# Performance work log

Hardware: AMD Instinct MI355X
Metric: run time of the kernel (lower is better)

The kernel has to match this reference:

```python
import jax, jax.numpy as jnp
import numpy as np

T = 64
NBITS_PSUM = 8
NBITS_ACC = 8
K = 2
EPS = 1e-5

def _binarize_ste(x):
    # sign binarization with straight-through estimator (torch code overwrites .data)
    s = jnp.where(x >= 0, 1.0, -1.0).astype(x.dtype)
    return x + jax.lax.stop_gradient(s - x)

def _binary_conv_psum(x, w):
    # x: [N,C,H,W], w: [O,C,3,3]. Binarized 3x3 conv (stride 1, pad 1) computed as
    # chunks of T products along the unrolled reduction dim, each partial sum
    # quantized to NBITS_PSUM bits with step K, final accumulator clipped to NBITS_ACC.
    N, C, H, W = x.shape
    O = w.shape[0]
    xb = _binarize_ste(x)
    wb = _binarize_ste(w)
    patches = jax.lax.conv_general_dilated_patches(
        xb, (3, 3), (1, 1), ((1, 1), (1, 1)),
        dimension_numbers=('NCHW', 'OIHW', 'NCHW'))  # [N, C*9, H, W], channel-major
    R = C * 9
    nch = R // T  # 2304 / 64 = 36 chunks
    p = patches.reshape(N, nch, T, H, W).transpose(1, 0, 2, 3, 4)  # [nch,N,T,H,W]
    wf = wb.reshape(O, nch, T).transpose(1, 0, 2)                   # [nch,O,T]
    qmax = 2 ** (NBITS_PSUM - 1) - 1
    step = float(K)

    def body(carry, xs):
        acc, reg = carry
        pc, wc = xs
        psum = jnp.einsum('nthw,ot->nohw', pc, wc)  # partial sum over T binary products
        q = jnp.clip(jnp.round(psum / step), -qmax - 1, qmax) * step
        q_ste = psum + jax.lax.stop_gradient(q - psum)  # STE through quantizer
        reg = reg + jnp.mean((q - psum) ** 2)  # quantization-error regularizer
        return (acc + q_ste, reg), None

    acc0 = jnp.zeros((N, O, H, W), x.dtype)
    (acc, reg), _ = jax.lax.scan(body, (acc0, jnp.zeros((), x.dtype)), (p, wf))
    amax = (2 ** (NBITS_ACC - 1) - 1) * step  # accumulator clipping
    return jnp.clip(acc, -amax, amax), reg

def _bn(x, gamma, beta):
    # BatchNorm2d in training mode (batch statistics)
    m = jnp.mean(x, (0, 2, 3), keepdims=True)
    v = jnp.var(x, (0, 2, 3), keepdims=True)
    return (x - m) * jax.lax.rsqrt(v + EPS) * gamma[None, :, None, None] + beta[None, :, None, None]

def setup_inputs():
    key = jax.random.key(0)
    k1, k2, k3 = jax.random.split(key, 3)
    N, C, H, W = 32, 256, 32, 32
    return {
        'x0': jax.random.normal(k1, (N, C, H, W), jnp.float32),
        'reg0': jnp.zeros((), jnp.float32),
        'w1': jax.random.normal(k2, (C, C, 3, 3), jnp.float32),
        'gamma1': jnp.ones((C,), jnp.float32),
        'beta1': jnp.zeros((C,), jnp.float32),
        'w2': jax.random.normal(k3, (C, C, 3, 3), jnp.float32),
        'gamma2': jnp.ones((C,), jnp.float32),
        'beta2': jnp.zeros((C,), jnp.float32),
    }

def reference(x0, reg0, w1, gamma1, beta1, w2, gamma2, beta2):
    residual = x0
    out, r1 = _binary_conv_psum(x0, w1)
    reg = reg0 + r1
    out = _bn(out, gamma1, beta1)
    out = jnp.clip(out, -1.0, 1.0)  # Hardtanh
    out, r2 = _binary_conv_psum(out, w2)
    reg = reg + r2
    out = out + residual  # downsample is None
    reg = reg + r2        # faithful to original: conv2's r is added again after residual
    out = _bn(out, gamma2, beta2)
    out = jnp.clip(out, -1.0, 1.0)  # Hardtanh (do_bntan=True)
    return out, reg
```

## Files before the change

kernel.cpp:

```cpp
#include <hip/hip_runtime.h>

typedef unsigned long long u64;
typedef __attribute__((ext_vector_type(4)))  int i32x4;
typedef __attribute__((ext_vector_type(16))) int i32x16;

#define NPIX   32768
#define OCH    256
#define NCH    36

#define AROWS  196
#define ALDS   (AROWS * 256)
#define BLDS   8192
#define GLDS   (ALDS + 3 * BLDS)

__device__ __forceinline__ void gload16(const void* g, void* l) {
  __builtin_amdgcn_global_load_lds(
      (const __attribute__((address_space(1))) unsigned*)g,
      (__attribute__((address_space(3))) unsigned*)l, 16, 0, 0);
}

__global__ void bb_prep(const float* wa, const float* wb, u64* Wbits,
                        signed char* B, float* st, u64* masks) {
  int blk = blockIdx.x, t = threadIdx.x;
  if (blk == 0) {
    for (int i = t; i < 1024; i += 256) st[i] = 0.f;
    for (int id = t; id < 9 * NCH; id += 256) {
      int cls = id / NCH, ck = id % NCH;
      int ch = cls / 3, cw = cls % 3;
      u64 m = 0;
      for (int b = 0; b < 64; ++b) {
        int r = ck * 64 + b, tap = r % 9, kh = tap / 3, kw = tap % 3;
        bool oob = (ch == 0 && kh == 0) || (ch == 2 && kh == 2) ||
                   (cw == 0 && kw == 0) || (cw == 2 && kw == 2);
        if (!oob) m |= (u64)1 << b;
      }
      masks[id] = m;
    }
  } else if (blk <= 4608) {
    int word = (((blk - 1) << 8) + t) >> 6;
    int ln = t & 63;
    const float* src = (word < OCH * NCH) ? wa : wb;
    int r = word % (OCH * NCH);
    u64 bits = __ballot(src[(size_t)r * 64 + ln] >= 0.f);
    int l = word / (OCH * NCH);
    int o = r / NCH, ck = r % NCH;
    if (ln == 0) Wbits[(size_t)l * OCH * NCH + (size_t)ck * OCH + o] = bits;
  } else {
    int tid = ((blk - 4609) << 8) + t;
    int l = tid >= 589824;
    int r = l ? tid - 589824 : tid;
    const float* src = l ? wb : wa;
    float v = src[r];
    int tp = r % 9, oc9 = r / 9;
    int c = oc9 & 255, o = oc9 >> 8;
    B[(((size_t)(l * 9 + tp) * 256 + o) << 8) + c] = (v >= 0.f) ? 1 : -1;
  }
}

__global__ __launch_bounds__(256) void bb_xbits(const float* __restrict__ x,
                                                u64* __restrict__ Sb,
                                                signed char* __restrict__ A) {
  __shared__ float xt[256][33];
  int n = blockIdx.x >> 5, h = blockIdx.x & 31;
  int t = threadIdx.x;
  int w = t & 31, cg = t >> 5;
  for (int k = 0; k < 32; ++k) {
    int c = k * 8 + cg;
    xt[c][w] = x[((size_t)((n * 256 + c) * 32 + h) << 5) + w];
  }
  __syncthreads();
  int ln = t & 63, wv = t >> 6;
  int c2 = wv * 64 + ln;
  for (int w2 = 0; w2 < 32; ++w2) {
    bool s = xt[c2][w2] >= 0.f;
    u64 bits = __ballot(s);
    int px = (n * 32 + h) * 32 + w2;
    A[(size_t)px * 256 + c2] = s ? 1 : -1;
    if (ln == 0) Sb[(size_t)px * 4 + wv] = bits;
  }
}

__global__ __launch_bounds__(256, 2) void bb_gemm(const signed char* __restrict__ A,
                                                  const signed char* __restrict__ B,
                                                  short* __restrict__ dst) {
  extern __shared__ signed char sm[];
  int t = threadIdx.x, wv = t >> 6, ln = t & 63;
  int lw = ln & 31, hk = ln >> 5;
  int px0 = blockIdx.x << 7;
  int oc0 = blockIdx.y << 7;

  const signed char* Abase = A + (size_t)(px0 - 33) * 256;
  #pragma unroll
  for (int i = 0; i < 13; ++i) {
    int c = i * 4 + wv;
    if (c < 49) {
      int u = c * 64 + ln;
      int row = u >> 4, p = u & 15;
      gload16(Abase + (size_t)row * 256 + (((p ^ (row & 7)) << 4)),
              &sm[c * 1024]);
    }
  }

  #define STAGE_B(bufi, ks) do {                                              \
    int tp_ = (ks) >> 2, cb_ = (ks) & 3;                                      \
    const signed char* Bb_ = B + ((size_t)tp_ << 16) + (size_t)oc0 * 256      \
                               + (cb_ << 6);                                  \
    _Pragma("unroll")                                                         \
    for (int i_ = 0; i_ < 2; ++i_) {                                          \
      int c_ = wv * 2 + i_;                                                   \
      int u_ = c_ * 64 + ln;                                                  \
      int row_ = u_ >> 2, p_ = u_ & 3;                                        \
      gload16(Bb_ + (size_t)row_ * 256 + (((p_ ^ ((row_ >> 1) & 3)) << 4)),   \
              &sm[ALDS + (bufi) * BLDS + c_ * 1024]);                         \
    }                                                                         \
  } while (0)

  STAGE_B(0, 0);
  STAGE_B(1, 1);
  asm volatile("s_waitcnt vmcnt(2)" ::: "memory");
  __builtin_amdgcn_s_barrier();

  int wm = wv >> 1, wn = wv & 1;
  int arow0 = 33 + (wm << 6) + lw;
  int brow0 = (wn << 6) + lw;
  i32x16 acc00 = {0,0,0,0,0,0,0,0,0,0,0,0,0,0,0,0};
  i32x16 acc01 = acc00, acc10 = acc00, acc11 = acc00;

  for (int ks = 0; ks < 36; ++ks) {
    if (ks + 2 < 36) STAGE_B((ks + 2) % 3, ks + 2);
    int tp = ks >> 2, cb = ks & 3;
    int dpx = (tp / 3 - 1) * 32 + (tp % 3 - 1);
    int r0 = arow0 + dpx, r1 = r0 + 32;
    int q0 = brow0, q1 = brow0 + 32;
    const signed char* Bl = sm + ALDS + (ks % 3) * BLDS;
    __builtin_amdgcn_s_setprio(1);
    #pragma unroll
    for (int k32 = 0; k32 < 2; ++k32) {
      int sa = cb * 4 + k32 * 2 + hk;
      int sb = k32 * 2 + hk;
      i32x4 a0 = *(const i32x4*)(sm + r0 * 256 + ((sa ^ (r0 & 7)) << 4));
      i32x4 a1 = *(const i32x4*)(sm + r1 * 256 + ((sa ^ (r1 & 7)) << 4));
      i32x4 b0 = *(const i32x4*)(Bl + q0 * 64 + ((sb ^ ((q0 >> 1) & 3)) << 4));
      i32x4 b1 = *(const i32x4*)(Bl + q1 * 64 + ((sb ^ ((q1 >> 1) & 3)) << 4));
      acc00 = __builtin_amdgcn_mfma_i32_32x32x32_i8(a0, b0, acc00, 0, 0, 0);
      acc01 = __builtin_amdgcn_mfma_i32_32x32x32_i8(a0, b1, acc01, 0, 0, 0);
      acc10 = __builtin_amdgcn_mfma_i32_32x32x32_i8(a1, b0, acc10, 0, 0, 0);
      acc11 = __builtin_amdgcn_mfma_i32_32x32x32_i8(a1, b1, acc11, 0, 0, 0);
    }
    __builtin_amdgcn_s_setprio(0);
    if (ks < 34) asm volatile("s_waitcnt vmcnt(2)" ::: "memory");
    else         asm volatile("s_waitcnt vmcnt(0)" ::: "memory");
    __builtin_amdgcn_s_barrier();
  }
  #undef STAGE_B

  int px0w = px0 + (wm << 6), oc0w = oc0 + (wn << 6);
  int rbase = hk << 2;
  #pragma unroll
  for (int r = 0; r < 16; ++r) {
    int m = (r & 3) + ((r >> 2) << 3) + rbase;
    size_t row0 = ((size_t)(px0w + m)) << 8;
    size_t row1 = ((size_t)(px0w + 32 + m)) << 8;
    int v;
    v = acc00[r]; v = v < -254 ? -254 : (v > 254 ? 254 : v);
    dst[row0 + oc0w + lw] = (short)v;
    v = acc01[r]; v = v < -254 ? -254 : (v > 254 ? 254 : v);
    dst[row0 + oc0w + 32 + lw] = (short)v;
    v = acc10[r]; v = v < -254 ? -254 : (v > 254 ? 254 : v);
    dst[row1 + oc0w + lw] = (short)v;
    v = acc11[r]; v = v < -254 ? -254 : (v > 254 ? 254 : v);
    dst[row1 + oc0w + 32 + lw] = (short)v;
  }
}

__global__ __launch_bounds__(256) void bb_bconv(const u64* __restrict__ Sb,
                                                const u64* __restrict__ Wb,
                                                const u64* __restrict__ masks,
                                                short* __restrict__ dst) {
  __shared__ u64 spread[256];
  __shared__ u64 pw[16][NCH];
  __shared__ u64 mm[16][NCH];
  __shared__ int pm[16][NCH];
  __shared__ int pxl[16];
  int t = threadIdx.x;
  {
    u64 v = 0;
    for (int k = 0; k < 8; ++k) if (t & (1 << k)) v |= (u64)1 << (9 * k);
    spread[t] = v;
  }
  __syncthreads();
  for (int id = t; id < 16 * NCH; id += 256) {
    int p = id / NCH, ck = id % NCH;
    int gp = blockIdx.x * 16 + p;
    int n = gp / 124, r = gp % 124;
    int h, w;
    if (r < 32)      { h = 0;      w = r;      }
    else if (r < 64) { h = 31;     w = r - 32; }
    else if (r < 94) { h = r - 63; w = 0;      }
    else             { h = r - 93; w = 31;     }
    int cls = (h == 0 ? 0 : (h == 31 ? 2 : 1)) * 3 + (w == 0 ? 0 : (w == 31 ? 2 : 1));
    if (ck == 0) pxl[p] = ((n * 32 + h) << 5) + w;
    int base9 = ck % 9;
    u64 acc = 0;
    for (int tap = 0; tap < 9; ++tap) {
      int b0 = tap - base9; if (b0 < 0) b0 += 9;
      int nh = h + tap / 3 - 1, nw = w + tap % 3 - 1;
      if ((unsigned)nh <= 31u && (unsigned)nw <= 31u) {
        int run = (b0 == 0) ? 8 : 7;
        int c0 = (ck * 64 + b0) / 9;
        const u64* rp = Sb + ((size_t)((n * 32 + nh) * 32 + nw) << 2);
        int wi = c0 >> 6, sh = c0 & 63;
        u64 v = rp[wi] >> sh;
        if (sh + run > 64) v |= rp[wi + 1] << (64 - sh);
        v &= (run == 8) ? 0xFFull : 0x7Full;
        acc |= spread[(int)v] << b0;
      }
    }
    pw[p][ck] = acc;
    u64 m = masks[cls * NCH + ck];
    mm[p][ck] = m;
    pm[p][ck] = __popcll(m);
  }
  __syncthreads();
  int oc = t;
  int acc[16];
  #pragma unroll
  for (int p = 0; p < 16; ++p) acc[p] = 0;
  for (int i = 0; i < NCH; ++i) {
    u64 wr = Wb[(size_t)i * OCH + oc];
    #pragma unroll
    for (int p = 0; p < 16; ++p) {
      int d = __popcll((pw[p][i] ^ wr) & mm[p][i]);
      int ps = pm[p][i] - 2 * d;
      acc[p] += ps + (ps & 1) * ((ps & 2) - 1);
    }
  }
  #pragma unroll
  for (int p = 0; p < 16; ++p) {
    int v = acc[p];
    v = v < -254 ? -254 : (v > 254 ? 254 : v);
    dst[(size_t)pxl[p] * OCH + oc] = (short)v;
  }
}

__global__ void bb_stats1(const short* v16, float* st) {
  int t = threadIdx.x;
  const short* base = v16 + (size_t)blockIdx.x * 128 * OCH;
  int s = 0; float q = 0.f;
  for (int r = 0; r < 128; ++r) {
    int v = base[r * OCH + t];
    s += v; q += (float)(v * v);
  }
  atomicAdd(&st[t], (float)s);
  atomicAdd(&st[256 + t], q);
}

__global__ void bb_xbits2(const short* v16, const float* st,
                          const float* g, const float* b, u64* Sb,
                          signed char* A) {
  int wave = (blockIdx.x * blockDim.x + threadIdx.x) >> 6;
  int ln = threadIdx.x & 63;
  int wrd = wave & 3, px0 = (wave >> 2) * 32;
  int oc = wrd * 64 + ln;
  float mu = st[oc] * (1.f / 32768.f);
  float va = st[256 + oc] * (1.f / 32768.f) - mu * mu;
  float rs = rsqrtf(va + 1e-5f);
  float gg = g[oc], bb = b[oc];
  for (int j = 0; j < 32; ++j) {
    float bn = ((float)v16[(size_t)(px0 + j) * OCH + oc] - mu) * rs * gg + bb;
    bool s = bn >= 0.f;
    u64 bits = __ballot(s);
    A[(size_t)(px0 + j) * 256 + oc] = s ? 1 : -1;
    if (ln == 0) Sb[(size_t)(px0 + j) * 4 + wrd] = bits;
  }
}

__global__ __launch_bounds__(256) void bb_stats2t(const short* __restrict__ pre16,
                                                  const float* __restrict__ x0,
                                                  float* st) {
  __shared__ float xt[32][257];
  int blk = blockIdx.x;
  int n = blk >> 5, h = blk & 31;
  int t = threadIdx.x;
  int w = t & 31, og = t >> 5;
  for (int k = 0; k < 32; ++k) {
    int oc = og * 32 + k;
    xt[w][oc] = x0[((size_t)(n * 256 + oc) * 32 + h) * 32 + w];
  }
  __syncthreads();
  int oc = t;
  size_t pb = (size_t)blk * 32 * OCH + oc;
  float s = 0.f, q = 0.f;
  for (int w2 = 0; w2 < 32; ++w2) {
    float v = (float)pre16[pb + (size_t)w2 * OCH] + xt[w2][oc];
    s += v; q += v * v;
  }
  atomicAdd(&st[512 + oc], s);
  atomicAdd(&st[768 + oc], q);
}

__global__ __launch_bounds__(256) void bb_fint(const short* __restrict__ pre16,
                                               const float* __restrict__ x0,
                                               const float* st, const float* g,
                                               const float* b, const float* r0,
                                               float* __restrict__ out) {
  __shared__ float xt[32][257];
  int blk = blockIdx.x;
  int n = blk >> 5, h = blk & 31;
  int t = threadIdx.x;
  int w = t & 31, og = t >> 5;
  for (int k = 0; k < 32; ++k) {
    int oc = og * 32 + k;
    xt[w][oc] = x0[((size_t)(n * 256 + oc) * 32 + h) * 32 + w];
  }
  __syncthreads();
  int oc = t;
  float mu = st[512 + oc] * (1.f / 32768.f);
  float va = st[768 + oc] * (1.f / 32768.f) - mu * mu;
  float rs = rsqrtf(va + 1e-5f);
  float gg = g[oc], bb = b[oc];
  size_t pb = (size_t)blk * 32 * OCH + oc;
  for (int w2 = 0; w2 < 32; ++w2) {
    float v = (float)pre16[pb + (size_t)w2 * OCH] + xt[w2][oc];
    v = (v - mu) * rs * gg + bb;
    xt[w2][oc] = fminf(fmaxf(v, -1.f), 1.f);
  }
  __syncthreads();
  for (int k = 0; k < 32; ++k) {
    int oc2 = og * 32 + k;
    out[((size_t)(n * 256 + oc2) * 32 + h) * 32 + w] = xt[w][oc2];
  }
  if (blk == 0 && t == 0) out[8388608] = r0[0] + 8.625f;
}

extern "C" void kernel_launch(void* const* d_in, const int* in_sizes, int n_in,
                              void* d_out, int out_size, void* d_ws, size_t ws_size,
                              hipStream_t stream) {
  const float* x0   = (const float*)d_in[0];
  const float* reg0 = (const float*)d_in[1];
  const float* w1   = (const float*)d_in[2];
  const float* g1   = (const float*)d_in[3];
  const float* b1   = (const float*)d_in[4];
  const float* w2   = (const float*)d_in[5];
  const float* g2   = (const float*)d_in[6];
  const float* b2   = (const float*)d_in[7];

  char* ws = (char*)d_ws;
  u64*   Wbits = (u64*)(ws);
  u64*   masks = (u64*)(ws + 147456);
  float* st    = (float*)(ws + 151552);
  u64*   Sb    = (u64*)(ws + 155648);
  signed char* Bi8 = (signed char*)(ws + 1204224);
  signed char* Ai8 = (signed char*)(ws + 2383872) + 32768;
  short* v16   = (short*)(ws + 10838016);

  bb_prep   <<<9217, 256, 0, stream>>>(w1, w2, Wbits, Bi8, st, masks);
  bb_xbits  <<<1024, 256, 0, stream>>>(x0, Sb, Ai8);
  bb_gemm   <<<dim3(256, 2), 256, GLDS, stream>>>(Ai8, Bi8, v16);
  bb_bconv  <<<248,  256, 0, stream>>>(Sb, Wbits, masks, v16);
  bb_stats1 <<<256,  256, 0, stream>>>(v16, st);
  bb_xbits2 <<<1024, 256, 0, stream>>>(v16, st, g1, b1, Sb, Ai8);
  bb_gemm   <<<dim3(256, 2), 256, GLDS, stream>>>(Ai8, Bi8 + 589824, v16);
  bb_bconv  <<<248,  256, 0, stream>>>(Sb, Wbits + OCH * NCH, masks, v16);
  bb_stats2t<<<1024, 256, 0, stream>>>(v16, x0, st);
  bb_fint   <<<1024, 256, 0, stream>>>(v16, x0, st, g2, b2, reg0, (float*)d_out);
}
```

Measured before the change: 308.0 us.

## Load GEMM B operand directly from global in MFMA-ready layout, drop LDS staging

The weight (B) matrix is now written by the prep kernel in a fragment-ordered layout so each lane can load its 16-byte MFMA operand straight from global memory. The triple-buffered LDS staging of B, its barriers and waitcnts are removed from the GEMM loop, which shrinks shared memory to the A tile and raises the occupancy hint to 3 blocks. This removes per-step synchronisation and LDS traffic, but B reads now go through L1/L2 with latency that is no longer explicitly prefetched, which may stall MFMAs.

New measurement: 320.0 us. 3.9% more time.

```diff
diff --git a/kernel.cpp b/kernel.cpp
--- a/kernel.cpp
+++ b/kernel.cpp
@@ -10,8 +10,6 @@
 
 #define AROWS  196
 #define ALDS   (AROWS * 256)
-#define BLDS   8192
-#define GLDS   (ALDS + 3 * BLDS)
 
 __device__ __forceinline__ void gload16(const void* g, void* l) {
   __builtin_amdgcn_global_load_lds(
@@ -53,7 +51,9 @@
     float v = src[r];
     int tp = r % 9, oc9 = r / 9;
     int c = oc9 & 255, o = oc9 >> 8;
-    B[(((size_t)(l * 9 + tp) * 256 + o) << 8) + c] = (v >= 0.f) ? 1 : -1;
+    int cb = c >> 6, s = (c >> 4) & 3, j = c & 15;
+    B[(((size_t)((l * 9 + tp) * 16 + cb * 4 + s)) << 12) + (o << 4) + j] =
+        (v >= 0.f) ? 1 : -1;
   }
 }
 
@@ -80,7 +80,7 @@
   }
 }
 
-__global__ __launch_bounds__(256, 2) void bb_gemm(const signed char* __restrict__ A,
+__global__ __launch_bounds__(256, 3) void bb_gemm(const signed char* __restrict__ A,
                                                   const signed char* __restrict__ B,
                                                   short* __restrict__ dst) {
   extern __shared__ signed char sm[];
@@ -100,59 +100,34 @@
               &sm[c * 1024]);
     }
   }
-
-  #define STAGE_B(bufi, ks) do {                                              \
-    int tp_ = (ks) >> 2, cb_ = (ks) & 3;                                      \
-    const signed char* Bb_ = B + ((size_t)tp_ << 16) + (size_t)oc0 * 256      \
-                               + (cb_ << 6);                                  \
-    _Pragma("unroll")                                                         \
-    for (int i_ = 0; i_ < 2; ++i_) {                                          \
-      int c_ = wv * 2 + i_;                                                   \
-      int u_ = c_ * 64 + ln;                                                  \
-      int row_ = u_ >> 2, p_ = u_ & 3;                                        \
-      gload16(Bb_ + (size_t)row_ * 256 + (((p_ ^ ((row_ >> 1) & 3)) << 4)),   \
-              &sm[ALDS + (bufi) * BLDS + c_ * 1024]);                         \
-    }                                                                         \
-  } while (0)
-
-  STAGE_B(0, 0);
-  STAGE_B(1, 1);
-  asm volatile("s_waitcnt vmcnt(2)" ::: "memory");
+  asm volatile("s_waitcnt vmcnt(0)" ::: "memory");
   __builtin_amdgcn_s_barrier();
 
   int wm = wv >> 1, wn = wv & 1;
   int arow0 = 33 + (wm << 6) + lw;
-  int brow0 = (wn << 6) + lw;
+  const signed char* Bw = B + (((size_t)(oc0 + (wn << 6) + lw)) << 4);
   i32x16 acc00 = {0,0,0,0,0,0,0,0,0,0,0,0,0,0,0,0};
   i32x16 acc01 = acc00, acc10 = acc00, acc11 = acc00;
 
+  #pragma unroll 4
   for (int ks = 0; ks < 36; ++ks) {
-    if (ks + 2 < 36) STAGE_B((ks + 2) % 3, ks + 2);
     int tp = ks >> 2, cb = ks & 3;
     int dpx = (tp / 3 - 1) * 32 + (tp % 3 - 1);
     int r0 = arow0 + dpx, r1 = r0 + 32;
-    int q0 = brow0, q1 = brow0 + 32;
-    const signed char* Bl = sm + ALDS + (ks % 3) * BLDS;
-    __builtin_amdgcn_s_setprio(1);
     #pragma unroll
     for (int k32 = 0; k32 < 2; ++k32) {
       int sa = cb * 4 + k32 * 2 + hk;
-      int sb = k32 * 2 + hk;
+      size_t bb = ((size_t)(tp * 16 + cb * 4 + k32 * 2 + hk)) << 12;
       i32x4 a0 = *(const i32x4*)(sm + r0 * 256 + ((sa ^ (r0 & 7)) << 4));
       i32x4 a1 = *(const i32x4*)(sm + r1 * 256 + ((sa ^ (r1 & 7)) << 4));
-      i32x4 b0 = *(const i32x4*)(Bl + q0 * 64 + ((sb ^ ((q0 >> 1) & 3)) << 4));
-      i32x4 b1 = *(const i32x4*)(Bl + q1 * 64 + ((sb ^ ((q1 >> 1) & 3)) << 4));
+      i32x4 b0 = *(const i32x4*)(Bw + bb);
+      i32x4 b1 = *(const i32x4*)(Bw + bb + (32 << 4));
       acc00 = __builtin_amdgcn_mfma_i32_32x32x32_i8(a0, b0, acc00, 0, 0, 0);
       acc01 = __builtin_amdgcn_mfma_i32_32x32x32_i8(a0, b1, acc01, 0, 0, 0);
       acc10 = __builtin_amdgcn_mfma_i32_32x32x32_i8(a1, b0, acc10, 0, 0, 0);
       acc11 = __builtin_amdgcn_mfma_i32_32x32x32_i8(a1, b1, acc11, 0, 0, 0);
     }
-    __builtin_amdgcn_s_setprio(0);
-    if (ks < 34) asm volatile("s_waitcnt vmcnt(2)" ::: "memory");
-    else         asm volatile("s_waitcnt vmcnt(0)" ::: "memory");
-    __builtin_amdgcn_s_barrier();
-  }
-  #undef STAGE_B
+  }
 
   int px0w = px0 + (wm << 6), oc0w = oc0 + (wn << 6);
   int rbase = hk << 2;
@@ -356,11 +331,11 @@
 
   bb_prep   <<<9217, 256, 0, stream>>>(w1, w2, Wbits, Bi8, st, masks);
   bb_xbits  <<<1024, 256, 0, stream>>>(x0, Sb, Ai8);
-  bb_gemm   <<<dim3(256, 2), 256, GLDS, stream>>>(Ai8, Bi8, v16);
+  bb_gemm   <<<dim3(256, 2), 256, ALDS, stream>>>(Ai8, Bi8, v16);
   bb_bconv  <<<248,  256, 0, stream>>>(Sb, Wbits, masks, v16);
   bb_stats1 <<<256,  256, 0, stream>>>(v16, st);
   bb_xbits2 <<<1024, 256, 0, stream>>>(v16, st, g1, b1, Sb, Ai8);
-  bb_gemm   <<<dim3(256, 2), 256, GLDS, stream>>>(Ai8, Bi8 + 589824, v16);
+  bb_gemm   <<<dim3(256, 2), 256, ALDS, stream>>>(Ai8, Bi8 + 589824, v16);
   bb_bconv  <<<248,  256, 0, stream>>>(Sb, Wbits + OCH * NCH, masks, v16);
   bb_stats2t<<<1024, 256, 0, stream>>>(v16, x0, st);
   bb_fint   <<<1024, 256, 0, stream>>>(v16, x0, st, g2, b2, reg0, (float*)d_out);
```

## Merge prep with xbits, and fuse interior GEMM with border bconv into one launch

Applied to the files above, without the earlier changes.

Folds the input binarization into the weight-prep kernel and combines the int8 MFMA GEMM and the border-pixel popcount conv into one kernel, with block ranges selecting the role. The GEMM now skips storing border pixels so the two roles write disjoint outputs and can run concurrently. This removes three kernel launches and the serialization between GEMM and bconv. The cost is that bconv blocks now reserve the large GEMM LDS allocation, which may limit their occupancy, and the prep kernel carries the xt shared array for every block.

New measurement: 283.4 us. -8.0%, faster.

```diff
diff --git a/kernel.cpp b/kernel.cpp
--- a/kernel.cpp
+++ b/kernel.cpp
@@ -19,8 +19,16 @@
       (__attribute__((address_space(3))) unsigned*)l, 16, 0, 0);
 }
 
-__global__ void bb_prep(const float* wa, const float* wb, u64* Wbits,
-                        signed char* B, float* st, u64* masks) {
+__global__ __launch_bounds__(256) void bb_pre(const float* __restrict__ wa,
+                                              const float* __restrict__ wb,
+                                              const float* __restrict__ x,
+                                              u64* __restrict__ Wbits,
+                                              signed char* __restrict__ B,
+                                              float* __restrict__ st,
+                                              u64* __restrict__ masks,
+                                              u64* __restrict__ Sb,
+                                              signed char* __restrict__ A) {
+  __shared__ float xt[256][33];
   int blk = blockIdx.x, t = threadIdx.x;
   if (blk == 0) {
     for (int i = t; i < 1024; i += 256) st[i] = 0.f;
@@ -45,7 +53,7 @@
     int l = word / (OCH * NCH);
     int o = r / NCH, ck = r % NCH;
     if (ln == 0) Wbits[(size_t)l * OCH * NCH + (size_t)ck * OCH + o] = bits;
-  } else {
+  } else if (blk <= 9216) {
     int tid = ((blk - 4609) << 8) + t;
     int l = tid >= 589824;
     int r = l ? tid - 589824 : tid;
@@ -54,144 +62,149 @@
     int tp = r % 9, oc9 = r / 9;
     int c = oc9 & 255, o = oc9 >> 8;
     B[(((size_t)(l * 9 + tp) * 256 + o) << 8) + c] = (v >= 0.f) ? 1 : -1;
-  }
-}
-
-__global__ __launch_bounds__(256) void bb_xbits(const float* __restrict__ x,
-                                                u64* __restrict__ Sb,
-                                                signed char* __restrict__ A) {
-  __shared__ float xt[256][33];
-  int n = blockIdx.x >> 5, h = blockIdx.x & 31;
-  int t = threadIdx.x;
-  int w = t & 31, cg = t >> 5;
-  for (int k = 0; k < 32; ++k) {
-    int c = k * 8 + cg;
-    xt[c][w] = x[((size_t)((n * 256 + c) * 32 + h) << 5) + w];
-  }
-  __syncthreads();
-  int ln = t & 63, wv = t >> 6;
-  int c2 = wv * 64 + ln;
-  for (int w2 = 0; w2 < 32; ++w2) {
-    bool s = xt[c2][w2] >= 0.f;
-    u64 bits = __ballot(s);
-    int px = (n * 32 + h) * 32 + w2;
-    A[(size_t)px * 256 + c2] = s ? 1 : -1;
-    if (ln == 0) Sb[(size_t)px * 4 + wv] = bits;
-  }
-}
-
-__global__ __launch_bounds__(256, 2) void bb_gemm(const signed char* __restrict__ A,
+  } else {
+    int bx = blk - 9217;
+    int n = bx >> 5, h = bx & 31;
+    int w = t & 31, cg = t >> 5;
+    for (int k = 0; k < 32; ++k) {
+      int c = k * 8 + cg;
+      xt[c][w] = x[((size_t)((n * 256 + c) * 32 + h) << 5) + w];
+    }
+    __syncthreads();
+    int ln = t & 63, wv = t >> 6;
+    int c2 = wv * 64 + ln;
+    for (int w2 = 0; w2 < 32; ++w2) {
+      bool s = xt[c2][w2] >= 0.f;
+      u64 bits = __ballot(s);
+      int px = (n * 32 + h) * 32 + w2;
+      A[(size_t)px * 256 + c2] = s ? 1 : -1;
+      if (ln == 0) Sb[(size_t)px * 4 + wv] = bits;
+    }
+  }
+}
+
+__global__ __launch_bounds__(256, 2) void bb_conv(const signed char* __restrict__ A,
                                                   const signed char* __restrict__ B,
+                                                  const u64* __restrict__ Sb,
+                                                  const u64* __restrict__ Wb,
+                                                  const u64* __restrict__ masks,
                                                   short* __restrict__ dst) {
   extern __shared__ signed char sm[];
-  int t = threadIdx.x, wv = t >> 6, ln = t & 63;
-  int lw = ln & 31, hk = ln >> 5;
-  int px0 = blockIdx.x << 7;
-  int oc0 = blockIdx.y << 7;
-
-  const signed char* Abase = A + (size_t)(px0 - 33) * 256;
-  #pragma unroll
-  for (int i = 0; i < 13; ++i) {
-    int c = i * 4 + wv;
-    if (c < 49) {
-      int u = c * 64 + ln;
-      int row = u >> 4, p = u & 15;
-      gload16(Abase + (size_t)row * 256 + (((p ^ (row & 7)) << 4)),
-              &sm[c * 1024]);
-    }
-  }
-
-  #define STAGE_B(bufi, ks) do {                                              \
-    int tp_ = (ks) >> 2, cb_ = (ks) & 3;                                      \
-    const signed char* Bb_ = B + ((size_t)tp_ << 16) + (size_t)oc0 * 256      \
-                               + (cb_ << 6);                                  \
-    _Pragma("unroll")                                                         \
-    for (int i_ = 0; i_ < 2; ++i_) {                                          \
-      int c_ = wv * 2 + i_;                                                   \
-      int u_ = c_ * 64 + ln;                                                  \
-      int row_ = u_ >> 2, p_ = u_ & 3;                                        \
-      gload16(Bb_ + (size_t)row_ * 256 + (((p_ ^ ((row_ >> 1) & 3)) << 4)),   \
-              &sm[ALDS + (bufi) * BLDS + c_ * 1024]);                         \
-    }                                                                         \
-  } while (0)
-
-  STAGE_B(0, 0);
-  STAGE_B(1, 1);
-  asm volatile("s_waitcnt vmcnt(2)" ::: "memory");
-  __builtin_amdgcn_s_barrier();
-
-  int wm = wv >> 1, wn = wv & 1;
-  int arow0 = 33 + (wm << 6) + lw;
-  int brow0 = (wn << 6) + lw;
-  i32x16 acc00 = {0,0,0,0,0,0,0,0,0,0,0,0,0,0,0,0};
-  i32x16 acc01 = acc00, acc10 = acc00, acc11 = acc00;
-
-  for (int ks = 0; ks < 36; ++ks) {
-    if (ks + 2 < 36) STAGE_B((ks + 2) % 3, ks + 2);
-    int tp = ks >> 2, cb = ks & 3;
-    int dpx = (tp / 3 - 1) * 32 + (tp % 3 - 1);
-    int r0 = arow0 + dpx, r1 = r0 + 32;
-    int q0 = brow0, q1 = brow0 + 32;
-    const signed char* Bl = sm + ALDS + (ks % 3) * BLDS;
-    __builtin_amdgcn_s_setprio(1);
+  int bx = blockIdx.x, t = threadIdx.x;
+  if (bx < 512) {
+    int wv = t >> 6, ln = t & 63;
+    int lw = ln & 31, hk = ln >> 5;
+    int px0 = (bx >> 1) << 7;
+    int oc0 = (bx & 1) << 7;
+
+    const signed char* Abase = A + (size_t)(px0 - 33) * 256;
     #pragma unroll
-    for (int k32 = 0; k32 < 2; ++k32) {
-      int sa = cb * 4 + k32 * 2 + hk;
-      int sb = k32 * 2 + hk;
-      i32x4 a0 = *(const i32x4*)(sm + r0 * 256 + ((sa ^ (r0 & 7)) << 4));
-      i32x4 a1 = *(const i32x4*)(sm + r1 * 256 + ((sa ^ (r1 & 7)) << 4));
-      i32x4 b0 = *(const i32x4*)(Bl + q0 * 64 + ((sb ^ ((q0 >> 1) & 3)) << 4));
-      i32x4 b1 = *(const i32x4*)(Bl + q1 * 64 + ((sb ^ ((q1 >> 1) & 3)) << 4));
-      acc00 = __builtin_amdgcn_mfma_i32_32x32x32_i8(a0, b0, acc00, 0, 0, 0);
-      acc01 = __builtin_amdgcn_mfma_i32_32x32x32_i8(a0, b1, acc01, 0, 0, 0);
-      acc10 = __builtin_amdgcn_mfma_i32_32x32x32_i8(a1, b0, acc10, 0, 0, 0);
-      acc11 = __builtin_amdgcn_mfma_i32_32x32x32_i8(a1, b1, acc11, 0, 0, 0);
-    }
-    __builtin_amdgcn_s_setprio(0);
-    if (ks < 34) asm volatile("s_waitcnt vmcnt(2)" ::: "memory");
-    else         asm volatile("s_waitcnt vmcnt(0)" ::: "memory");
+    for (int i = 0; i < 13; ++i) {
+      int c = i * 4 + wv;
+      if (c < 49) {
+        int u = c * 64 + ln;
+        int row = u >> 4, p = u & 15;
+        gload16(Abase + (size_t)row * 256 + (((p ^ (row & 7)) << 4)),
+                &sm[c * 1024]);
+      }
+    }
+
+    #define STAGE_B(bufi, ks) do {                                            \
+      int tp_ = (ks) >> 2, cb_ = (ks) & 3;                                    \
+      const signed char* Bb_ = B + ((size_t)tp_ << 16) + (size_t)oc0 * 256    \
+                                 + (cb_ << 6);                                \
+      _Pragma("unroll")                                                       \
+      for (int i_ = 0; i_ < 2; ++i_) {                                        \
+        int c_ = wv * 2 + i_;                                                 \
+        int u_ = c_ * 64 + ln;                                                \
+        int row_ = u_ >> 2, p_ = u_ & 3;                                      \
+        gload16(Bb_ + (size_t)row_ * 256 + (((p_ ^ ((row_ >> 1) & 3)) << 4)), \
+                &sm[ALDS + (bufi) * BLDS + c_ * 1024]);                       \
+      }                                                                       \
+    } while (0)
+
+    STAGE_B(0, 0);
+    STAGE_B(1, 1);
+    asm volatile("s_waitcnt vmcnt(2)" ::: "memory");
     __builtin_amdgcn_s_barrier();
-  }
-  #undef STAGE_B
-
-  int px0w = px0 + (wm << 6), oc0w = oc0 + (wn << 6);
-  int rbase = hk << 2;
-  #pragma unroll
-  for (int r = 0; r < 16; ++r) {
-    int m = (r & 3) + ((r >> 2) << 3) + rbase;
-    size_t row0 = ((size_t)(px0w + m)) << 8;
-    size_t row1 = ((size_t)(px0w + 32 + m)) << 8;
-    int v;
-    v = acc00[r]; v = v < -254 ? -254 : (v > 254 ? 254 : v);
-    dst[row0 + oc0w + lw] = (short)v;
-    v = acc01[r]; v = v < -254 ? -254 : (v > 254 ? 254 : v);
-    dst[row0 + oc0w + 32 + lw] = (short)v;
-    v = acc10[r]; v = v < -254 ? -254 : (v > 254 ? 254 : v);
-    dst[row1 + oc0w + lw] = (short)v;
-    v = acc11[r]; v = v < -254 ? -254 : (v > 254 ? 254 : v);
-    dst[row1 + oc0w + 32 + lw] = (short)v;
-  }
-}
-
-__global__ __launch_bounds__(256) void bb_bconv(const u64* __restrict__ Sb,
-                                                const u64* __restrict__ Wb,
-                                                const u64* __restrict__ masks,
-                                                short* __restrict__ dst) {
-  __shared__ u64 spread[256];
-  __shared__ u64 pw[16][NCH];
-  __shared__ u64 mm[16][NCH];
-  __shared__ int pm[16][NCH];
-  __shared__ int pxl[16];
-  int t = threadIdx.x;
+
+    int wm = wv >> 1, wn = wv & 1;
+    int arow0 = 33 + (wm << 6) + lw;
+    int brow0 = (wn << 6) + lw;
+    i32x16 acc00 = {0,0,0,0,0,0,0,0,0,0,0,0,0,0,0,0};
+    i32x16 acc01 = acc00, acc10 = acc00, acc11 = acc00;
+
+    for (int ks = 0; ks < 36; ++ks) {
+      if (ks + 2 < 36) STAGE_B((ks + 2) % 3, ks + 2);
+      int tp = ks >> 2, cb = ks & 3;
+      int dpx = (tp / 3 - 1) * 32 + (tp % 3 - 1);
+      int r0 = arow0 + dpx, r1 = r0 + 32;
+      int q0 = brow0, q1 = brow0 + 32;
+      const signed char* Bl = sm + ALDS + (ks % 3) * BLDS;
+      __builtin_amdgcn_s_setprio(1);
+      #pragma unroll
+      for (int k32 = 0; k32 < 2; ++k32) {
+        int sa = cb * 4 + k32 * 2 + hk;
+        int sb = k32 * 2 + hk;
+        i32x4 a0 = *(const i32x4*)(sm + r0 * 256 + ((sa ^ (r0 & 7)) << 4));
+        i32x4 a1 = *(const i32x4*)(sm + r1 * 256 + ((sa ^ (r1 & 7)) << 4));
+        i32x4 b0 = *(const i32x4*)(Bl + q0 * 64 + ((sb ^ ((q0 >> 1) & 3)) << 4));
+        i32x4 b1 = *(const i32x4*)(Bl + q1 * 64 + ((sb ^ ((q1 >> 1) & 3)) << 4));
+        acc00 = __builtin_amdgcn_mfma_i32_32x32x32_i8(a0, b0, acc00, 0, 0, 0);
+        acc01 = __builtin_amdgcn_mfma_i32_32x32x32_i8(a0, b1, acc01, 0, 0, 0);
+        acc10 = __builtin_amdgcn_mfma_i32_32x32x32_i8(a1, b0, acc10, 0, 0, 0);
+        acc11 = __builtin_amdgcn_mfma_i32_32x32x32_i8(a1, b1, acc11, 0, 0, 0);
+      }
+      __builtin_amdgcn_s_setprio(0);
+      if (ks < 34) asm volatile("s_waitcnt vmcnt(2)" ::: "memory");
+      else         asm volatile("s_waitcnt vmcnt(0)" ::: "memory");
+      __builtin_amdgcn_s_barrier();
+    }
+    #undef STAGE_B
+
+    int px0w = px0 + (wm << 6), oc0w = oc0 + (wn << 6);
+    int rbase = hk << 2;
+    int h0 = (px0w >> 5) & 31, h1 = ((px0w + 32) >> 5) & 31;
+    bool i0 = (h0 >= 1) && (h0 <= 30);
+    bool i1 = (h1 >= 1) && (h1 <= 30);
+    #pragma unroll
+    for (int r = 0; r < 16; ++r) {
+      int m = (r & 3) + ((r >> 2) << 3) + rbase;
+      bool wok = (m >= 1) && (m <= 30);
+      size_t row0 = ((size_t)(px0w + m)) << 8;
+      size_t row1 = ((size_t)(px0w + 32 + m)) << 8;
+      int v;
+      if (i0 && wok) {
+        v = acc00[r]; v = v < -254 ? -254 : (v > 254 ? 254 : v);
+        dst[row0 + oc0w + lw] = (short)v;
+        v = acc01[r]; v = v < -254 ? -254 : (v > 254 ? 254 : v);
+        dst[row0 + oc0w + 32 + lw] = (short)v;
+      }
+      if (i1 && wok) {
+        v = acc10[r]; v = v < -254 ? -254 : (v > 254 ? 254 : v);
+        dst[row1 + oc0w + lw] = (short)v;
+        v = acc11[r]; v = v < -254 ? -254 : (v > 254 ? 254 : v);
+        dst[row1 + oc0w + 32 + lw] = (short)v;
+      }
+    }
+    return;
+  }
+
+  u64* spread = (u64*)sm;
+  u64* pw     = spread + 256;
+  u64* mm     = pw + 16 * NCH;
+  int* pm     = (int*)(mm + 16 * NCH);
+  int* pxl    = pm + 16 * NCH;
   {
     u64 v = 0;
     for (int k = 0; k < 8; ++k) if (t & (1 << k)) v |= (u64)1 << (9 * k);
     spread[t] = v;
   }
   __syncthreads();
+  int bb = bx - 512;
   for (int id = t; id < 16 * NCH; id += 256) {
     int p = id / NCH, ck = id % NCH;
-    int gp = blockIdx.x * 16 + p;
+    int gp = bb * 16 + p;
     int n = gp / 124, r = gp % 124;
     int h, w;
     if (r < 32)      { h = 0;      w = r;      }
@@ -216,10 +229,10 @@
         acc |= spread[(int)v] << b0;
       }
     }
-    pw[p][ck] = acc;
+    pw[p * NCH + ck] = acc;
     u64 m = masks[cls * NCH + ck];
-    mm[p][ck] = m;
-    pm[p][ck] = __popcll(m);
+    mm[p * NCH + ck] = m;
+    pm[p * NCH + ck] = __popcll(m);
   }
   __syncthreads();
   int oc = t;
@@ -230,8 +243,8 @@
     u64 wr = Wb[(size_t)i * OCH + oc];
     #pragma unroll
     for (int p = 0; p < 16; ++p) {
-      int d = __popcll((pw[p][i] ^ wr) & mm[p][i]);
-      int ps = pm[p][i] - 2 * d;
+      int d = __popcll((pw[p * NCH + i] ^ wr) & mm[p * NCH + i]);
+      int ps = pm[p * NCH + i] - 2 * d;
       acc[p] += ps + (ps & 1) * ((ps & 2) - 1);
     }
   }
@@ -354,14 +367,13 @@
   signed char* Ai8 = (signed char*)(ws + 2383872) + 32768;
   short* v16   = (short*)(ws + 10838016);
 
-  bb_prep   <<<9217, 256, 0, stream>>>(w1, w2, Wbits, Bi8, st, masks);
-  bb_xbits  <<<1024, 256, 0, stream>>>(x0, Sb, Ai8);
-  bb_gemm   <<<dim3(256, 2), 256, GLDS, stream>>>(Ai8, Bi8, v16);
-  bb_bconv  <<<248,  256, 0, stream>>>(Sb, Wbits, masks, v16);
-  bb_stats1 <<<256,  256, 0, stream>>>(v16, st);
+  bb_pre    <<<10241, 256, 0, stream>>>(w1, w2, x0, Wbits, Bi8, st, masks,
+                                        Sb, Ai8);
+  bb_conv   <<<760, 256, GLDS, stream>>>(Ai8, Bi8, Sb, Wbits, masks, v16);
+  bb_stats1 <<<256, 256, 0, stream>>>(v16, st);
   bb_xbits2 <<<1024, 256, 0, stream>>>(v16, st, g1, b1, Sb, Ai8);
-  bb_gemm   <<<dim3(256, 2), 256, GLDS, stream>>>(Ai8, Bi8 + 589824, v16);
-  bb_bconv  <<<248,  256, 0, stream>>>(Sb, Wbits + OCH * NCH, masks, v16);
+  bb_conv   <<<760, 256, GLDS, stream>>>(Ai8, Bi8 + 589824, Sb,
+                                         Wbits + OCH * NCH, masks, v16);
   bb_stats2t<<<1024, 256, 0, stream>>>(v16, x0, st);
   bb_fint   <<<1024, 256, 0, stream>>>(v16, x0, st, g2, b2, reg0, (float*)d_out);
 }
```
